# Kernel tuning notes

Measured on AMD Instinct MI355X. Metric: run time of the kernel, lower is better.

Reference implementation:

```python
import jax, jax.numpy as jnp
import numpy as np

EPS = 1e-07
GAMMA = 2.0
LAMBDA_DISCO = 1000.0


def _binary_entropy(target, output):
    x = jnp.clip(output, EPS, 1.0 - EPS)
    return -target * jnp.log(x) - (1.0 - target) * jnp.log(1.0 - x)


def _focal_bce(target, output, y_class, y_pred_class):
    yc = y_class[:, 0]
    ypc = y_pred_class[:, 0]
    y_pred = output[:, 0]
    bce = _binary_entropy(target, y_pred)
    m = jnp.mean(ypc)
    s = jnp.std(ypc)  # population std, matches tf.math.reduce_std
    norm = jnp.clip((ypc - m) / (2.0 * s) + 0.5, 0.0, 1.0)
    class_weight_factor = ((1.0 - yc) * norm) ** GAMMA
    norm_factor = jnp.sum(1.0 - yc) / jnp.sum(class_weight_factor)
    return class_weight_factor * bce * norm_factor


def _distance_corr(var_1, var_2, w, power):
    # pairwise |x_i - x_j| distance matrices [N, N]
    amat = jnp.abs(var_1[:, None] - var_1[None, :])
    bmat = jnp.abs(var_2[:, None] - var_2[None, :])
    amatavg = jnp.mean(amat * w, axis=1)
    bmatavg = jnp.mean(bmat * w, axis=1)
    # double centering (tile layout: minuend_1[i,j]=avg[j], minuend_2[i,j]=avg[i])
    Amat = amat - amatavg[None, :] - amatavg[:, None] + jnp.mean(amatavg * w)
    Bmat = bmat - bmatavg[None, :] - bmatavg[:, None] + jnp.mean(bmatavg * w)
    ABavg = jnp.abs(jnp.mean(Amat * Bmat * w, axis=1))
    AAavg = jnp.mean(Amat * Amat * w, axis=1)
    BBavg = jnp.mean(Bmat * Bmat * w, axis=1)
    mAB = jnp.mean(ABavg * w)
    mAA = jnp.mean(AAavg * w)
    mBB = jnp.mean(BBavg * w)
    if power == 1:
        dCorr = mAB / jnp.sqrt(jnp.abs(mAA * mBB) + 1e-12)
    elif power == 2:
        dCorr = mAB ** 2 / (jnp.abs(mAA * mBB) + 1e-12)
    else:
        dCorr = (mAB / jnp.sqrt(mAA * mBB) + 1e-12) ** power
    dCorr = jnp.where(jnp.isnan(dCorr), 0.0, dCorr)
    dCorr = jnp.where(dCorr < 0.0, 0.0, dCorr)
    return dCorr


def setup_inputs() -> dict:
    N = 4096
    key = jax.random.key(0)
    ks = jax.random.split(key, 6)
    target = jnp.round(jax.random.uniform(ks[0], (N,), dtype=jnp.float32))
    output = jax.random.uniform(ks[1], (N, 1), dtype=jnp.float32, minval=0.02, maxval=0.98)
    y_class = jnp.round(jax.random.uniform(ks[2], (N, 1), dtype=jnp.float32))
    y_pred_class = jax.random.uniform(ks[3], (N, 1), dtype=jnp.float32, minval=0.02, maxval=0.98)
    var_1 = jax.random.normal(ks[4], (N,), dtype=jnp.float32) * 20.0 + 100.0  # mass-like
    var_2 = jax.random.uniform(ks[5], (N,), dtype=jnp.float32)  # classifier-output-like
    normedweight = jnp.ones((N,), dtype=jnp.float32)  # sums to N as required
    return {"target": target, "output": output, "y_class": y_class,
            "y_pred_class": y_pred_class, "var_1": var_1, "var_2": var_2,
            "normedweight": normedweight, "power": 1}


def reference(target, output, y_class, y_pred_class, var_1, var_2, normedweight, power):
    focal = _focal_bce(target, output, y_class, y_pred_class)
    dcorr = _distance_corr(var_1, var_2, normedweight, power)
    return jnp.mean(focal) + LAMBDA_DISCO * dcorr
```

## Files before the change

### kernel.cpp

```cpp
#include <hip/hip_runtime.h>
#include <math.h>

#define N 4096
#define HALF 2048
#define RPB 32
#define LANES 16
#define NRB (N / RPB)
#define NPASS (NRB * 2)
#define FEPS 1e-7f


__device__ __forceinline__ double block_reduce(double v) {
    __shared__ double buf[4];
    int tid = threadIdx.x;
    #pragma unroll
    for (int o = 32; o > 0; o >>= 1) v += __shfl_down(v, o, 64);
    __syncthreads();
    if ((tid & 63) == 0) buf[tid >> 6] = v;
    __syncthreads();
    return buf[0] + buf[1] + buf[2] + buf[3];
}

__global__ __launch_bounds__(256) void k1(
        const float* __restrict__ target,
        const float* __restrict__ output,
        const float* __restrict__ y_class,
        const float* __restrict__ y_pred_class,
        const float* __restrict__ v1,
        const float* __restrict__ v2,
        const float* __restrict__ w,
        double* __restrict__ wd,
        int* __restrict__ counter,
        float* __restrict__ rowA_p,
        float* __restrict__ rowB_p) {
    int tid = threadIdx.x;
    int b = blockIdx.x;

    if (b == NPASS) {
        if (tid == 0) *counter = 0;
        double s_ypc = 0.0, s_ypc2 = 0.0, s_yc = 0.0;
        for (int i = tid; i < N; i += 256) {
            float ypc = y_pred_class[i];
            s_ypc  += (double)ypc;
            s_ypc2 += (double)ypc * (double)ypc;
            s_yc   += (double)y_class[i];
        }
        double t_ypc  = block_reduce(s_ypc);
        double t_ypc2 = block_reduce(s_ypc2);
        double t_yc   = block_reduce(s_yc);

        __shared__ float  sm, sinv2s;
        __shared__ double s_sum1myc;
        if (tid == 0) {
            double m   = t_ypc / (double)N;
            double var = t_ypc2 / (double)N - m * m;
            double sd  = sqrt(var > 0.0 ? var : 0.0);
            sm     = (float)m;
            sinv2s = (float)(1.0 / (2.0 * sd));
            s_sum1myc = (double)N - t_yc;
        }
        __syncthreads();

        float m = sm, inv2s = sinv2s;
        double s_cwf = 0.0, s_cwfb = 0.0;
        for (int i = tid; i < N; i += 256) {
            float yc  = y_class[i];
            float ypc = y_pred_class[i];
            float nrm = (ypc - m) * inv2s + 0.5f;
            nrm = fminf(fmaxf(nrm, 0.0f), 1.0f);
            float c1  = (1.0f - yc) * nrm;
            float cwf = c1 * c1;
            float x = fminf(fmaxf(output[i], FEPS), 1.0f - FEPS);
            float t = target[i];
            float bce = -t * logf(x) - (1.0f - t) * logf(1.0f - x);
            s_cwf  += (double)cwf;
            s_cwfb += (double)cwf * (double)bce;
        }
        double t_cwf  = block_reduce(s_cwf);
        double t_cwfb = block_reduce(s_cwfb);
        if (tid == 0) wd[0] = t_cwfb * (s_sum1myc / t_cwf) / (double)N;
        return;
    }

    int h  = b & 1;
    int rb = b >> 1;
    int j0 = h * HALF;
    __shared__ float s1[HALF], s2[HALF], sw[HALF];
    for (int t = tid * 4; t < HALF; t += 1024) {
        *(float4*)&s1[t] = *(const float4*)&v1[j0 + t];
        *(float4*)&s2[t] = *(const float4*)&v2[j0 + t];
        *(float4*)&sw[t] = *(const float4*)&w [j0 + t];
    }
    __syncthreads();

    int lane = tid & (LANES - 1);
    int g    = tid >> 4;
    int i0   = rb * RPB + g * 2;
    float a0 = v1[i0],     a1 = v1[i0 + 1];
    float b0 = v2[i0],     b1 = v2[i0 + 1];
    float sa0 = 0.f, sa1 = 0.f, sb0 = 0.f, sb1 = 0.f;
    #pragma unroll 8
    for (int k = 0; k < HALF / (LANES * 4); ++k) {
        int j = 4 * lane + 64 * k;
        float4 x1 = *(const float4*)&s1[j];
        float4 x2 = *(const float4*)&s2[j];
        float4 xw = *(const float4*)&sw[j];
        #define P1(c)                                  \
        {                                              \
            sa0 = fmaf(fabsf(a0 - x1.c), xw.c, sa0);   \
            sa1 = fmaf(fabsf(a1 - x1.c), xw.c, sa1);   \
            sb0 = fmaf(fabsf(b0 - x2.c), xw.c, sb0);   \
            sb1 = fmaf(fabsf(b1 - x2.c), xw.c, sb1);   \
        }
        P1(x) P1(y) P1(z) P1(w)
        #undef P1
    }
    #pragma unroll
    for (int o = 1; o < LANES; o <<= 1) {
        sa0 += __shfl_xor(sa0, o, LANES);
        sa1 += __shfl_xor(sa1, o, LANES);
        sb0 += __shfl_xor(sb0, o, LANES);
        sb1 += __shfl_xor(sb1, o, LANES);
    }
    if (lane == 0) {
        rowA_p[h * N + i0]     = sa0;
        rowA_p[h * N + i0 + 1] = sa1;
        rowB_p[h * N + i0]     = sb0;
        rowB_p[h * N + i0 + 1] = sb1;
    }
}

__global__ __launch_bounds__(256) void k2(
        const float* __restrict__ v1,
        const float* __restrict__ v2,
        const float* __restrict__ w,
        const float* __restrict__ rowA_p,
        const float* __restrict__ rowB_p,
        const double* __restrict__ wd,
        const int* __restrict__ power,
        int* __restrict__ counter,
        float* __restrict__ pABr,
        float* __restrict__ pAAr,
        float* __restrict__ pBBr,
        float* __restrict__ out) {
    __shared__ float s1[HALF], s2[HALF], sw[HALF], sav[HALF], sbv[HALF];
    int tid = threadIdx.x;
    int b = blockIdx.x;
    int h  = b & 1;
    int rb = b >> 1;
    int j0 = h * HALF;
    const float invN = 1.0f / (float)N;

    for (int t = tid * 4; t < HALF; t += 1024) {
        *(float4*)&s1[t] = *(const float4*)&v1[j0 + t];
        *(float4*)&s2[t] = *(const float4*)&v2[j0 + t];
        *(float4*)&sw[t] = *(const float4*)&w [j0 + t];
        float4 r0 = *(const float4*)&rowA_p[j0 + t];
        float4 r1 = *(const float4*)&rowA_p[N + j0 + t];
        float4 q0 = *(const float4*)&rowB_p[j0 + t];
        float4 q1 = *(const float4*)&rowB_p[N + j0 + t];
        float4 ra, rbv;
        ra.x  = (r0.x + r1.x) * invN;  ra.y  = (r0.y + r1.y) * invN;
        ra.z  = (r0.z + r1.z) * invN;  ra.w  = (r0.w + r1.w) * invN;
        rbv.x = (q0.x + q1.x) * invN;  rbv.y = (q0.y + q1.y) * invN;
        rbv.z = (q0.z + q1.z) * invN;  rbv.w = (q0.w + q1.w) * invN;
        *(float4*)&sav[t] = ra;
        *(float4*)&sbv[t] = rbv;
    }
    __syncthreads();

    double sgA = 0.0, sgB = 0.0;
    for (int i = tid; i < N; i += 256) {
        double wi = (double)w[i];
        sgA += (double)(rowA_p[i] + rowA_p[N + i]) * wi;
        sgB += (double)(rowB_p[i] + rowB_p[N + i]) * wi;
    }
    const double NN = (double)N * (double)N;
    float gA = (float)(block_reduce(sgA) / NN);
    float gB = (float)(block_reduce(sgB) / NN);

    int lane = tid & (LANES - 1);
    int g    = tid >> 4;
    int i0   = rb * RPB + g * 2;
    float a0 = v1[i0],   a1 = v1[i0 + 1];
    float e0 = v2[i0],   e1 = v2[i0 + 1];
    float cA0 = (rowA_p[i0]     + rowA_p[N + i0])     * invN - gA;
    float cA1 = (rowA_p[i0 + 1] + rowA_p[N + i0 + 1]) * invN - gA;
    float cB0 = (rowB_p[i0]     + rowB_p[N + i0])     * invN - gB;
    float cB1 = (rowB_p[i0 + 1] + rowB_p[N + i0 + 1]) * invN - gB;

    float ab0 = 0.f, aa0 = 0.f, bb0 = 0.f;
    float ab1 = 0.f, aa1 = 0.f, bb1 = 0.f;
    #pragma unroll 4
    for (int k = 0; k < HALF / (LANES * 4); ++k) {
        int j = 4 * lane + 64 * k;
        float4 x1 = *(const float4*)&s1[j];
        float4 x2 = *(const float4*)&s2[j];
        float4 xw = *(const float4*)&sw[j];
        float4 xa = *(const float4*)&sav[j];
        float4 xb = *(const float4*)&sbv[j];
        #define P2(c)                                            \
        {                                                        \
            float Am0 = fabsf(a0 - x1.c) - xa.c - cA0;           \
            float Bm0 = fabsf(e0 - x2.c) - xb.c - cB0;           \
            float Am1 = fabsf(a1 - x1.c) - xa.c - cA1;           \
            float Bm1 = fabsf(e1 - x2.c) - xb.c - cB1;           \
            float Aw0 = Am0 * xw.c, Bw0 = Bm0 * xw.c;            \
            float Aw1 = Am1 * xw.c, Bw1 = Bm1 * xw.c;            \
            ab0 = fmaf(Aw0, Bm0, ab0);                           \
            aa0 = fmaf(Aw0, Am0, aa0);                           \
            bb0 = fmaf(Bw0, Bm0, bb0);                           \
            ab1 = fmaf(Aw1, Bm1, ab1);                           \
            aa1 = fmaf(Aw1, Am1, aa1);                           \
            bb1 = fmaf(Bw1, Bm1, bb1);                           \
        }
        P2(x) P2(y) P2(z) P2(w)
        #undef P2
    }
    #pragma unroll
    for (int o = 1; o < LANES; o <<= 1) {
        ab0 += __shfl_xor(ab0, o, LANES);
        aa0 += __shfl_xor(aa0, o, LANES);
        bb0 += __shfl_xor(bb0, o, LANES);
        ab1 += __shfl_xor(ab1, o, LANES);
        aa1 += __shfl_xor(aa1, o, LANES);
        bb1 += __shfl_xor(bb1, o, LANES);
    }
    if (lane == 0) {
        pABr[h * N + i0]     = ab0;
        pABr[h * N + i0 + 1] = ab1;
        pAAr[h * N + i0]     = aa0;
        pAAr[h * N + i0 + 1] = aa1;
        pBBr[h * N + i0]     = bb0;
        pBBr[h * N + i0 + 1] = bb1;
    }

    __shared__ int isLast;
    if (tid == 0) {
        __threadfence();
        int old = atomicAdd(counter, 1);
        isLast = (old == NPASS - 1);
    }
    __syncthreads();
    if (!isLast) return;
    __threadfence();

    double sab = 0.0, saa = 0.0, sbb = 0.0;
    for (int i = tid; i < N; i += 256) {
        double wi = (double)w[i];
        sab += fabs((double)(pABr[i] + pABr[N + i])) * wi;
        saa += (double)(pAAr[i] + pAAr[N + i]) * wi;
        sbb += (double)(pBBr[i] + pBBr[N + i]) * wi;
    }
    double tab = block_reduce(sab);
    double taa = block_reduce(saa);
    double tbb = block_reduce(sbb);
    if (tid == 0) {
        double mAB = tab / NN;
        double mAA = taa / NN;
        double mBB = tbb / NN;
        int p = power[0];
        double d;
        if (p == 1) {
            d = mAB / sqrt(fabs(mAA * mBB) + 1e-12);
        } else if (p == 2) {
            d = (mAB * mAB) / (fabs(mAA * mBB) + 1e-12);
        } else {
            d = pow(mAB / sqrt(mAA * mBB) + 1e-12, (double)p);
        }
        if (isnan(d)) d = 0.0;
        if (d < 0.0)  d = 0.0;
        out[0] = (float)(wd[0] + 1000.0 * d);
    }
}

extern "C" void kernel_launch(void* const* d_in, const int* in_sizes, int n_in,
                              void* d_out, int out_size, void* d_ws, size_t ws_size,
                              hipStream_t stream) {
    const float* target       = (const float*)d_in[0];
    const float* output       = (const float*)d_in[1];
    const float* y_class      = (const float*)d_in[2];
    const float* y_pred_class = (const float*)d_in[3];
    const float* var_1        = (const float*)d_in[4];
    const float* var_2        = (const float*)d_in[5];
    const float* normedweight = (const float*)d_in[6];
    const int*   power        = (const int*)d_in[7];
    float* out = (float*)d_out;

    char*   ws      = (char*)d_ws;
    double* wd      = (double*)ws;
    int*    counter = (int*)(ws + 16);
    float*  rowA_p  = (float*)(ws + 64);
    float*  rowB_p  = rowA_p + 2 * N;
    float*  pABr    = rowB_p + 2 * N;
    float*  pAAr    = pABr  + 2 * N;
    float*  pBBr    = pAAr  + 2 * N;

    k1<<<NPASS + 1, 256, 0, stream>>>(target, output, y_class, y_pred_class,
                                      var_1, var_2, normedweight, wd, counter,
                                      rowA_p, rowB_p);
    k2<<<NPASS, 256, 0, stream>>>(var_1, var_2, normedweight, rowA_p, rowB_p,
                                  wd, power, counter, pABr, pAAr, pBBr, out);
}
```

Baseline: 39.47 us.

## Fuse both passes into one cooperative kernel with grid sync

Merges the two kernels into a single cooperative launch of 256 blocks that each keep the full 4096-element vectors in shared memory, using a grid-wide sync between the row-mean pass and the centered-product pass. Each block handles 16 full rows instead of half-rows, so the partial-row combination and the redundant global-mean recomputation go away. Per-block partial sums are reduced locally, so the final reduction shrinks to 256 values. In exchange it uses 80 KB of shared memory per block, which lowers occupancy, and it pays for the cooperative launch and grid barrier.

New measurement: 115.4 us. 192% more time.

```diff
diff --git a/kernel.cpp b/kernel.cpp
--- a/kernel.cpp
+++ b/kernel.cpp
@@ -1,12 +1,12 @@
 #include <hip/hip_runtime.h>
+#include <hip/hip_cooperative_groups.h>
 #include <math.h>
 
+namespace cg = cooperative_groups;
+
 #define N 4096
-#define HALF 2048
-#define RPB 32
-#define LANES 16
-#define NRB (N / RPB)
-#define NPASS (NRB * 2)
+#define RPB 16
+#define NBLK 256
 #define FEPS 1e-7f
 
 
@@ -21,7 +21,7 @@
     return buf[0] + buf[1] + buf[2] + buf[3];
 }
 
-__global__ __launch_bounds__(256) void k1(
+__global__ __launch_bounds__(256) void fused(
         const float* __restrict__ target,
         const float* __restrict__ output,
         const float* __restrict__ y_class,
@@ -29,15 +29,31 @@
         const float* __restrict__ v1,
         const float* __restrict__ v2,
         const float* __restrict__ w,
+        const int* __restrict__ power,
+        int* __restrict__ counter,
+        float* __restrict__ rowA,
+        float* __restrict__ rowB,
+        double* __restrict__ pg,
+        double* __restrict__ pr,
         double* __restrict__ wd,
-        int* __restrict__ counter,
-        float* __restrict__ rowA_p,
-        float* __restrict__ rowB_p) {
+        float* __restrict__ out) {
+    cg::grid_group grid = cg::this_grid();
+    __shared__ float s1[N], s2[N], sw[N];
+    __shared__ float sav[N], sbv[N];
+    __shared__ float rsA[RPB], rsB[RPB];
     int tid = threadIdx.x;
-    int b = blockIdx.x;
-
-    if (b == NPASS) {
-        if (tid == 0) *counter = 0;
+    int b   = blockIdx.x;
+
+    if (b == 0 && tid == 0) *counter = 0;
+
+    for (int t = tid * 4; t < N; t += 1024) {
+        *(float4*)&s1[t] = *(const float4*)&v1[t];
+        *(float4*)&s2[t] = *(const float4*)&v2[t];
+        *(float4*)&sw[t] = *(const float4*)&w [t];
+    }
+    __syncthreads();
+
+    if (b == NBLK - 1) {
         double s_ypc = 0.0, s_ypc2 = 0.0, s_yc = 0.0;
         for (int i = tid; i < N; i += 256) {
             float ypc = y_pred_class[i];
@@ -79,29 +95,17 @@
         double t_cwf  = block_reduce(s_cwf);
         double t_cwfb = block_reduce(s_cwfb);
         if (tid == 0) wd[0] = t_cwfb * (s_sum1myc / t_cwf) / (double)N;
-        return;
-    }
-
-    int h  = b & 1;
-    int rb = b >> 1;
-    int j0 = h * HALF;
-    __shared__ float s1[HALF], s2[HALF], sw[HALF];
-    for (int t = tid * 4; t < HALF; t += 1024) {
-        *(float4*)&s1[t] = *(const float4*)&v1[j0 + t];
-        *(float4*)&s2[t] = *(const float4*)&v2[j0 + t];
-        *(float4*)&sw[t] = *(const float4*)&w [j0 + t];
-    }
-    __syncthreads();
-
-    int lane = tid & (LANES - 1);
-    int g    = tid >> 4;
-    int i0   = rb * RPB + g * 2;
-    float a0 = v1[i0],     a1 = v1[i0 + 1];
-    float b0 = v2[i0],     b1 = v2[i0 + 1];
+    }
+
+    int lane = tid & 31;
+    int g    = tid >> 5;
+    int i0   = b * RPB + g * 2;
+    float a0 = s1[i0], a1 = s1[i0 + 1];
+    float e0 = s2[i0], e1 = s2[i0 + 1];
     float sa0 = 0.f, sa1 = 0.f, sb0 = 0.f, sb1 = 0.f;
-    #pragma unroll 8
-    for (int k = 0; k < HALF / (LANES * 4); ++k) {
-        int j = 4 * lane + 64 * k;
+    #pragma unroll 4
+    for (int k = 0; k < N / (32 * 4); ++k) {
+        int j = 4 * lane + 128 * k;
         float4 x1 = *(const float4*)&s1[j];
         float4 x2 = *(const float4*)&s2[j];
         float4 xw = *(const float4*)&sw[j];
@@ -109,91 +113,65 @@
         {                                              \
             sa0 = fmaf(fabsf(a0 - x1.c), xw.c, sa0);   \
             sa1 = fmaf(fabsf(a1 - x1.c), xw.c, sa1);   \
-            sb0 = fmaf(fabsf(b0 - x2.c), xw.c, sb0);   \
-            sb1 = fmaf(fabsf(b1 - x2.c), xw.c, sb1);   \
+            sb0 = fmaf(fabsf(e0 - x2.c), xw.c, sb0);   \
+            sb1 = fmaf(fabsf(e1 - x2.c), xw.c, sb1);   \
         }
         P1(x) P1(y) P1(z) P1(w)
         #undef P1
     }
     #pragma unroll
-    for (int o = 1; o < LANES; o <<= 1) {
-        sa0 += __shfl_xor(sa0, o, LANES);
-        sa1 += __shfl_xor(sa1, o, LANES);
-        sb0 += __shfl_xor(sb0, o, LANES);
-        sb1 += __shfl_xor(sb1, o, LANES);
+    for (int o = 1; o < 32; o <<= 1) {
+        sa0 += __shfl_xor(sa0, o, 32);
+        sa1 += __shfl_xor(sa1, o, 32);
+        sb0 += __shfl_xor(sb0, o, 32);
+        sb1 += __shfl_xor(sb1, o, 32);
     }
     if (lane == 0) {
-        rowA_p[h * N + i0]     = sa0;
-        rowA_p[h * N + i0 + 1] = sa1;
-        rowB_p[h * N + i0]     = sb0;
-        rowB_p[h * N + i0 + 1] = sb1;
-    }
-}
-
-__global__ __launch_bounds__(256) void k2(
-        const float* __restrict__ v1,
-        const float* __restrict__ v2,
-        const float* __restrict__ w,
-        const float* __restrict__ rowA_p,
-        const float* __restrict__ rowB_p,
-        const double* __restrict__ wd,
-        const int* __restrict__ power,
-        int* __restrict__ counter,
-        float* __restrict__ pABr,
-        float* __restrict__ pAAr,
-        float* __restrict__ pBBr,
-        float* __restrict__ out) {
-    __shared__ float s1[HALF], s2[HALF], sw[HALF], sav[HALF], sbv[HALF];
-    int tid = threadIdx.x;
-    int b = blockIdx.x;
-    int h  = b & 1;
-    int rb = b >> 1;
-    int j0 = h * HALF;
+        rowA[i0] = sa0; rowA[i0 + 1] = sa1;
+        rowB[i0] = sb0; rowB[i0 + 1] = sb1;
+        rsA[g * 2] = sa0; rsA[g * 2 + 1] = sa1;
+        rsB[g * 2] = sb0; rsB[g * 2 + 1] = sb1;
+    }
+    __syncthreads();
+    if (tid == 0) {
+        double ga = 0.0, gb = 0.0;
+        #pragma unroll
+        for (int q = 0; q < RPB; ++q) {
+            double wq = (double)sw[b * RPB + q];
+            ga += (double)rsA[q] * wq;
+            gb += (double)rsB[q] * wq;
+        }
+        pg[b] = ga; pg[NBLK + b] = gb;
+    }
+    __threadfence();
+    grid.sync();
+    __threadfence();
+
+    const double NN = (double)N * (double)N;
+    float gA = (float)(block_reduce(pg[tid]) / NN);
+    float gB = (float)(block_reduce(pg[NBLK + tid]) / NN);
+
     const float invN = 1.0f / (float)N;
-
-    for (int t = tid * 4; t < HALF; t += 1024) {
-        *(float4*)&s1[t] = *(const float4*)&v1[j0 + t];
-        *(float4*)&s2[t] = *(const float4*)&v2[j0 + t];
-        *(float4*)&sw[t] = *(const float4*)&w [j0 + t];
-        float4 r0 = *(const float4*)&rowA_p[j0 + t];
-        float4 r1 = *(const float4*)&rowA_p[N + j0 + t];
-        float4 q0 = *(const float4*)&rowB_p[j0 + t];
-        float4 q1 = *(const float4*)&rowB_p[N + j0 + t];
-        float4 ra, rbv;
-        ra.x  = (r0.x + r1.x) * invN;  ra.y  = (r0.y + r1.y) * invN;
-        ra.z  = (r0.z + r1.z) * invN;  ra.w  = (r0.w + r1.w) * invN;
-        rbv.x = (q0.x + q1.x) * invN;  rbv.y = (q0.y + q1.y) * invN;
-        rbv.z = (q0.z + q1.z) * invN;  rbv.w = (q0.w + q1.w) * invN;
+    for (int t = tid * 4; t < N; t += 1024) {
+        float4 ra = *(const float4*)&rowA[t];
+        float4 rb = *(const float4*)&rowB[t];
+        ra.x *= invN; ra.y *= invN; ra.z *= invN; ra.w *= invN;
+        rb.x *= invN; rb.y *= invN; rb.z *= invN; rb.w *= invN;
         *(float4*)&sav[t] = ra;
-        *(float4*)&sbv[t] = rbv;
-    }
-    __syncthreads();
-
-    double sgA = 0.0, sgB = 0.0;
-    for (int i = tid; i < N; i += 256) {
-        double wi = (double)w[i];
-        sgA += (double)(rowA_p[i] + rowA_p[N + i]) * wi;
-        sgB += (double)(rowB_p[i] + rowB_p[N + i]) * wi;
-    }
-    const double NN = (double)N * (double)N;
-    float gA = (float)(block_reduce(sgA) / NN);
-    float gB = (float)(block_reduce(sgB) / NN);
-
-    int lane = tid & (LANES - 1);
-    int g    = tid >> 4;
-    int i0   = rb * RPB + g * 2;
-    float a0 = v1[i0],   a1 = v1[i0 + 1];
-    float e0 = v2[i0],   e1 = v2[i0 + 1];
-    float cA0 = (rowA_p[i0]     + rowA_p[N + i0])     * invN - gA;
-    float cA1 = (rowA_p[i0 + 1] + rowA_p[N + i0 + 1]) * invN - gA;
-    float cB0 = (rowB_p[i0]     + rowB_p[N + i0])     * invN - gB;
-    float cB1 = (rowB_p[i0 + 1] + rowB_p[N + i0 + 1]) * invN - gB;
+        *(float4*)&sbv[t] = rb;
+    }
+    __syncthreads();
+
+    float cA0 = sav[i0]     - gA;
+    float cA1 = sav[i0 + 1] - gA;
+    float cB0 = sbv[i0]     - gB;
+    float cB1 = sbv[i0 + 1] - gB;
 
     float ab0 = 0.f, aa0 = 0.f, bb0 = 0.f;
     float ab1 = 0.f, aa1 = 0.f, bb1 = 0.f;
     #pragma unroll 4
-    for (int k = 0; k < HALF / (LANES * 4); ++k) {
-        int j = 4 * lane + 64 * k;
+    for (int k = 0; k < N / (32 * 4); ++k) {
+        int j = 4 * lane + 128 * k;
         float4 x1 = *(const float4*)&s1[j];
         float4 x2 = *(const float4*)&s2[j];
         float4 xw = *(const float4*)&sw[j];
@@ -218,43 +196,41 @@
         #undef P2
     }
     #pragma unroll
-    for (int o = 1; o < LANES; o <<= 1) {
-        ab0 += __shfl_xor(ab0, o, LANES);
-        aa0 += __shfl_xor(aa0, o, LANES);
-        bb0 += __shfl_xor(bb0, o, LANES);
-        ab1 += __shfl_xor(ab1, o, LANES);
-        aa1 += __shfl_xor(aa1, o, LANES);
-        bb1 += __shfl_xor(bb1, o, LANES);
-    }
+    for (int o = 1; o < 32; o <<= 1) {
+        ab0 += __shfl_xor(ab0, o, 32);
+        aa0 += __shfl_xor(aa0, o, 32);
+        bb0 += __shfl_xor(bb0, o, 32);
+        ab1 += __shfl_xor(ab1, o, 32);
+        aa1 += __shfl_xor(aa1, o, 32);
+        bb1 += __shfl_xor(bb1, o, 32);
+    }
+    __shared__ double rd[3][RPB];
     if (lane == 0) {
-        pABr[h * N + i0]     = ab0;
-        pABr[h * N + i0 + 1] = ab1;
-        pAAr[h * N + i0]     = aa0;
-        pAAr[h * N + i0 + 1] = aa1;
-        pBBr[h * N + i0]     = bb0;
-        pBBr[h * N + i0 + 1] = bb1;
+        double w0 = (double)sw[i0], w1 = (double)sw[i0 + 1];
+        rd[0][g * 2] = fabs((double)ab0) * w0;  rd[0][g * 2 + 1] = fabs((double)ab1) * w1;
+        rd[1][g * 2] = (double)aa0 * w0;        rd[1][g * 2 + 1] = (double)aa1 * w1;
+        rd[2][g * 2] = (double)bb0 * w0;        rd[2][g * 2 + 1] = (double)bb1 * w1;
+    }
+    __syncthreads();
+    if (tid == 0) {
+        double tab = 0.0, taa = 0.0, tbb = 0.0;
+        #pragma unroll
+        for (int q = 0; q < RPB; ++q) { tab += rd[0][q]; taa += rd[1][q]; tbb += rd[2][q]; }
+        pr[b] = tab; pr[NBLK + b] = taa; pr[2 * NBLK + b] = tbb;
     }
 
     __shared__ int isLast;
     if (tid == 0) {
         __threadfence();
-        int old = atomicAdd(counter, 1);
-        isLast = (old == NPASS - 1);
+        isLast = (atomicAdd(counter, 1) == NBLK - 1);
     }
     __syncthreads();
     if (!isLast) return;
     __threadfence();
 
-    double sab = 0.0, saa = 0.0, sbb = 0.0;
-    for (int i = tid; i < N; i += 256) {
-        double wi = (double)w[i];
-        sab += fabs((double)(pABr[i] + pABr[N + i])) * wi;
-        saa += (double)(pAAr[i] + pAAr[N + i]) * wi;
-        sbb += (double)(pBBr[i] + pBBr[N + i]) * wi;
-    }
-    double tab = block_reduce(sab);
-    double taa = block_reduce(saa);
-    double tbb = block_reduce(sbb);
+    double tab = block_reduce(pr[tid]);
+    double taa = block_reduce(pr[NBLK + tid]);
+    double tbb = block_reduce(pr[2 * NBLK + tid]);
     if (tid == 0) {
         double mAB = tab / NN;
         double mAA = taa / NN;
@@ -290,15 +266,14 @@
     char*   ws      = (char*)d_ws;
     double* wd      = (double*)ws;
     int*    counter = (int*)(ws + 16);
-    float*  rowA_p  = (float*)(ws + 64);
-    float*  rowB_p  = rowA_p + 2 * N;
-    float*  pABr    = rowB_p + 2 * N;
-    float*  pAAr    = pABr  + 2 * N;
-    float*  pBBr    = pAAr  + 2 * N;
-
-    k1<<<NPASS + 1, 256, 0, stream>>>(target, output, y_class, y_pred_class,
-                                      var_1, var_2, normedweight, wd, counter,
-                                      rowA_p, rowB_p);
-    k2<<<NPASS, 256, 0, stream>>>(var_1, var_2, normedweight, rowA_p, rowB_p,
-                                  wd, power, counter, pABr, pAAr, pBBr, out);
+    double* pg      = (double*)(ws + 64);
+    double* pr      = (double*)(ws + 64 + 4096);
+    float*  rowA    = (float*)(ws + 64 + 4096 + 6144);
+    float*  rowB    = rowA + N;
+
+    void* args[] = { &target, &output, &y_class, &y_pred_class,
+                     &var_1, &var_2, &normedweight, &power,
+                     &counter, &rowA, &rowB, &pg, &pr, &wd, &out };
+    hipLaunchCooperativeKernel((const void*)fused, dim3(NBLK), dim3(256),
+                               args, 0, stream);
 }
```
